# Performance work log

Hardware: AMD Instinct MI355X
Metric: run time of the kernel (lower is better)

The kernel has to match this reference:

```python
import jax, jax.numpy as jnp
import numpy as np

N_NODES = 100000
N_EDGES = 3200000
IN_DIM = 512
HID = 256
N_CLASSES = 40


def spmm(edge_src, edge_dst, edge_w, h):
    # out[d] = sum_{e: dst[e]==d} w[e] * h[src[e]]   (COO sparse-dense matmul)
    msgs = h[edge_src] * edge_w[:, None]  # [E, F]
    return jax.ops.segment_sum(msgs, edge_dst, num_segments=N_NODES)


def setup_inputs() -> dict:
    key = jax.random.key(0)
    ks = jax.random.split(key, 20)
    inp = {
        "x": jax.random.normal(ks[0], (N_NODES, IN_DIM), dtype=jnp.float32),
        "edge_src": jax.random.randint(ks[1], (N_EDGES,), 0, N_NODES, dtype=jnp.int32),
        "edge_dst": jax.random.randint(ks[2], (N_EDGES,), 0, N_NODES, dtype=jnp.int32),
        "edge_w": jax.random.uniform(ks[3], (N_EDGES,), dtype=jnp.float32),
    }
    def lin(k, fi, fo):
        s = 1.0 / np.sqrt(fi)
        kw, kb = jax.random.split(k)
        return (jax.random.uniform(kw, (fi, fo), minval=-s, maxval=s, dtype=jnp.float32),
                jax.random.uniform(kb, (fo,), minval=-s, maxval=s, dtype=jnp.float32))
    inp["w1"], inp["b1"] = lin(ks[4], IN_DIM, HID)      # GCN layer 1
    inp["w2"], inp["b2"] = lin(ks[5], HID, HID)         # GCN layer 2
    inp["wc1"], inp["bc1"] = lin(ks[6], HID, 2 * HID)   # classifier MLP
    inp["wc2"], inp["bc2"] = lin(ks[7], 2 * HID, 2 * HID)
    inp["wc3"], inp["bc3"] = lin(ks[8], 2 * HID, 2 * HID)
    inp["wc4"], inp["bc4"] = lin(ks[9], 2 * HID, N_CLASSES)
    return inp


def reference(x, edge_src, edge_dst, edge_w, w1, b1, w2, b2,
              wc1, bc1, wc2, bc2, wc3, bc3, wc4, bc4):
    h = jax.nn.relu(spmm(edge_src, edge_dst, edge_w, x @ w1) + b1)
    # dropout rate = 0.0 -> identity
    h = spmm(edge_src, edge_dst, edge_w, h @ w2) + b2
    # node classifier MLP
    h = jax.nn.relu(h @ wc1 + bc1)
    h = jax.nn.relu(h @ wc2 + bc2)
    h = jax.nn.relu(h @ wc3 + bc3)
    logits = h @ wc4 + bc4
    return jax.nn.softmax(logits, axis=1)
```

## Files before the change

kernel.cpp:

```cpp
#include <hip/hip_runtime.h>
#include <math.h>

typedef __attribute__((ext_vector_type(8))) _Float16 f16x8;
typedef __attribute__((ext_vector_type(4))) float f32x4;
typedef __attribute__((ext_vector_type(8))) unsigned short ushort8;


__device__ __forceinline__ float bf2f(unsigned short u) {
    union { unsigned int i; float f; } x; x.i = ((unsigned int)u) << 16; return x.f;
}
__device__ __forceinline__ unsigned short f2bf(float f) {
    union { float f; unsigned int i; } x; x.f = f;
    unsigned int i = x.i;
    unsigned int r = (i + 0x7FFFu + ((i >> 16) & 1u)) >> 16;
    return (unsigned short)r;
}
__device__ __forceinline__ float h2f(unsigned short u) {
    _Float16 h; __builtin_memcpy(&h, &u, 2); return (float)h;
}
__device__ __forceinline__ unsigned short f2h(float f) {
    _Float16 h = (_Float16)f; unsigned short u; __builtin_memcpy(&u, &h, 2); return u;
}
__device__ __forceinline__ float ld1(const void* p, long i, bool bf) {
    return bf ? bf2f(((const unsigned short*)p)[i]) : ((const float*)p)[i];
}
__device__ __forceinline__ float4 ld4(const void* p, long i, bool bf) {
    if (bf) {
        ushort4 u = *(const ushort4*)((const unsigned short*)p + i);
        return make_float4(bf2f(u.x), bf2f(u.y), bf2f(u.z), bf2f(u.w));
    }
    return *(const float4*)((const float*)p + i);
}

__global__ void k_detect(const unsigned int* __restrict__ x, int* __restrict__ flag) {
    int t = threadIdx.x;
    int hits = 0;
    for (int i = 0; i < 64; i++) {
        unsigned int w = x[t * 64 + i];
        unsigned int e = (w >> 7) & 0xFF;
        hits += (e >= 0x70 && e <= 0x85) ? 1 : 0;
    }
    __shared__ int sh[256];
    sh[t] = hits;
    __syncthreads();
    for (int off = 128; off; off >>= 1) {
        if (t < off) sh[t] += sh[t + off];
        __syncthreads();
    }
    if (t == 0) *flag = (sh[0] > 8192) ? 1 : 0;
}


__global__ void k_hist(const int* __restrict__ dst, int E, int* __restrict__ counts) {
    int i = blockIdx.x * blockDim.x + threadIdx.x;
    if (i < E) atomicAdd(&counts[dst[i]], 1);
}

__global__ void k_scan_a(const int* __restrict__ counts, int N,
                         int* __restrict__ ex, int* __restrict__ bsums) {
    __shared__ int s[256];
    int t = threadIdx.x;
    int base = blockIdx.x * 1024;
    int v[4]; int sum = 0;
    #pragma unroll
    for (int j = 0; j < 4; j++) {
        int idx = base + t * 4 + j;
        v[j] = (idx < N) ? counts[idx] : 0;
        sum += v[j];
    }
    s[t] = sum;
    __syncthreads();
    for (int off = 1; off < 256; off <<= 1) {
        int x = (t >= off) ? s[t - off] : 0;
        __syncthreads();
        s[t] += x;
        __syncthreads();
    }
    int run = (t > 0) ? s[t - 1] : 0;
    #pragma unroll
    for (int j = 0; j < 4; j++) {
        int idx = base + t * 4 + j;
        if (idx < N) ex[idx] = run;
        run += v[j];
    }
    if (t == 255) bsums[blockIdx.x] = s[255];
}

__global__ void k_scan_b(int* __restrict__ bsums, int nb) {
    __shared__ int s[256];
    int t = threadIdx.x;
    s[t] = (t < nb) ? bsums[t] : 0;
    __syncthreads();
    for (int off = 1; off < 256; off <<= 1) {
        int x = (t >= off) ? s[t - off] : 0;
        __syncthreads();
        s[t] += x;
        __syncthreads();
    }
    if (t < nb) bsums[t] = (t > 0) ? s[t - 1] : 0;
}

__global__ void k_scan_c(const int* __restrict__ ex, const int* __restrict__ bsums,
                         int N, int E, int* __restrict__ row_ptr) {
    int i = blockIdx.x * blockDim.x + threadIdx.x;
    if (i < N) row_ptr[i] = ex[i] + bsums[i >> 10];
    if (i == 0) row_ptr[N] = E;
}

__global__ void k_scatter(const int* __restrict__ src, const int* __restrict__ dst,
                          const void* __restrict__ ewin, const int* __restrict__ dflag,
                          const int* __restrict__ row_ptr, int* __restrict__ cursor,
                          int E, int* __restrict__ es, float* __restrict__ ew) {
    int i = blockIdx.x * blockDim.x + threadIdx.x;
    if (i >= E) return;
    bool bf = (*dflag != 0);
    int d = dst[i];
    int p = row_ptr[d] + atomicAdd(&cursor[d], 1);
    es[p] = src[i];
    ew[p] = ld1(ewin, i, bf);
}


__global__ __launch_bounds__(256) void k_gemm(
    const void* __restrict__ A, const void* __restrict__ W, const void* __restrict__ bias,
    void* __restrict__ C, int M, int K, int N,
    int a_kind, int c_mode, int act, const int* __restrict__ dflag)
{
    const bool inbf = (*dflag != 0);
    const int  a_mode = (a_kind == 2) ? 2 : (inbf ? 1 : 0);
    const bool a_lo = (a_mode == 0);
    const bool b_lo = !inbf;

    __shared__ _Float16 Ah[128][40];
    __shared__ _Float16 Al[128][40];
    __shared__ _Float16 Bh[128][40];
    __shared__ _Float16 Bl[128][40];

    const int t  = threadIdx.x;
    const int m0 = blockIdx.y * 128;
    const int n0 = blockIdx.x * 128;

    const int lane = t & 63;
    const int wv   = t >> 6;
    const int wm   = (wv & 1) * 64;
    const int wn   = (wv >> 1) * 64;
    const int lr   = lane & 15;
    const int lk   = (lane >> 4) * 8;

    f32x4 acc[4][4];
    const f32x4 vzero = {0.f, 0.f, 0.f, 0.f};
    #pragma unroll
    for (int i = 0; i < 4; i++)
        #pragma unroll
        for (int j = 0; j < 4; j++) acc[i][j] = vzero;

    const int  ar  = t >> 1;
    const int  ak  = (t & 1) * 16;
    const long agm = (long)(m0 + ar);

    const int nq = t & 31;
    const int kq = t >> 5;
    const int gn = n0 + nq * 4;

    for (int k0 = 0; k0 < K; k0 += 32) {
        #pragma unroll
        for (int c = 0; c < 2; c++) {
            long base = agm * K + k0 + ak + c * 8;
            if (a_mode == 2) {
                uint4 raw = make_uint4(0, 0, 0, 0);
                if (agm < M) raw = *(const uint4*)((const unsigned short*)A + base);
                *(uint4*)&Ah[ar][ak + c * 8] = raw;
            } else if (a_mode == 1) {
                union { unsigned short u[8]; uint4 q; } r;
                r.q = make_uint4(0, 0, 0, 0);
                if (agm < M) r.q = *(const uint4*)((const unsigned short*)A + base);
                union { _Float16 h[8]; uint4 q; } H;
                #pragma unroll
                for (int e = 0; e < 8; e++) H.h[e] = (_Float16)bf2f(r.u[e]);
                *(uint4*)&Ah[ar][ak + c * 8] = H.q;
            } else {
                float4 v0 = make_float4(0.f, 0.f, 0.f, 0.f), v1 = v0;
                if (agm < M) {
                    v0 = *(const float4*)((const float*)A + base);
                    v1 = *(const float4*)((const float*)A + base + 4);
                }
                float f[8] = {v0.x, v0.y, v0.z, v0.w, v1.x, v1.y, v1.z, v1.w};
                union { _Float16 h[8]; uint4 q; } H, L;
                #pragma unroll
                for (int e = 0; e < 8; e++) {
                    _Float16 hh = (_Float16)f[e];
                    H.h[e] = hh;
                    L.h[e] = (_Float16)(f[e] - (float)hh);
                }
                *(uint4*)&Ah[ar][ak + c * 8] = H.q;
                *(uint4*)&Al[ar][ak + c * 8] = L.q;
            }
        }
        {
            float w[4][4];
            #pragma unroll
            for (int i = 0; i < 4; i++) {
                float4 v = make_float4(0.f, 0.f, 0.f, 0.f);
                if (gn < N) v = ld4(W, (long)(k0 + kq * 4 + i) * N + gn, inbf);
                w[i][0] = v.x; w[i][1] = v.y; w[i][2] = v.z; w[i][3] = v.w;
            }
            #pragma unroll
            for (int j = 0; j < 4; j++) {
                union { _Float16 h[4]; uint2 q; } H, L;
                #pragma unroll
                for (int i = 0; i < 4; i++) {
                    _Float16 hh = (_Float16)w[i][j];
                    H.h[i] = hh;
                    if (b_lo) L.h[i] = (_Float16)(w[i][j] - (float)hh);
                }
                *(uint2*)&Bh[nq * 4 + j][kq * 4] = H.q;
                if (b_lo) *(uint2*)&Bl[nq * 4 + j][kq * 4] = L.q;
            }
        }
        __syncthreads();

        f16x8 ah[4], bh[4];
        #pragma unroll
        for (int f = 0; f < 4; f++) {
            ah[f] = *(const f16x8*)&Ah[wm + f * 16 + lr][lk];
            bh[f] = *(const f16x8*)&Bh[wn + f * 16 + lr][lk];
        }
        #pragma unroll
        for (int i = 0; i < 4; i++)
            #pragma unroll
            for (int j = 0; j < 4; j++)
                acc[i][j] = __builtin_amdgcn_mfma_f32_16x16x32_f16(ah[i], bh[j], acc[i][j], 0, 0, 0);
        if (a_lo) {
            f16x8 al[4];
            #pragma unroll
            for (int f = 0; f < 4; f++) al[f] = *(const f16x8*)&Al[wm + f * 16 + lr][lk];
            #pragma unroll
            for (int i = 0; i < 4; i++)
                #pragma unroll
                for (int j = 0; j < 4; j++)
                    acc[i][j] = __builtin_amdgcn_mfma_f32_16x16x32_f16(al[i], bh[j], acc[i][j], 0, 0, 0);
        }
        if (b_lo) {
            f16x8 bl[4];
            #pragma unroll
            for (int f = 0; f < 4; f++) bl[f] = *(const f16x8*)&Bl[wn + f * 16 + lr][lk];
            #pragma unroll
            for (int i = 0; i < 4; i++)
                #pragma unroll
                for (int j = 0; j < 4; j++)
                    acc[i][j] = __builtin_amdgcn_mfma_f32_16x16x32_f16(ah[i], bl[j], acc[i][j], 0, 0, 0);
        }
        __syncthreads();
    }

    const bool has_bias = (bias != nullptr);
    const int  rbase = (lane >> 4) * 4;
    #pragma unroll
    for (int j = 0; j < 4; j++) {
        int col = n0 + wn + j * 16 + lr;
        if (col >= N) continue;
        float bv = has_bias ? ld1(bias, col, inbf) : 0.f;
        #pragma unroll
        for (int i = 0; i < 4; i++) {
            #pragma unroll
            for (int r = 0; r < 4; r++) {
                int row = m0 + wm + i * 16 + rbase + r;
                if (row < M) {
                    float v = acc[i][j][r] + bv;
                    if (act) v = fmaxf(v, 0.f);
                    if (c_mode == 2) ((unsigned short*)C)[(long)row * N + col] = f2h(v);
                    else             ((float*)C)[(long)row * N + col] = v;
                }
            }
        }
    }
}


__global__ __launch_bounds__(256) void k_spmm(
    const unsigned short* __restrict__ sup, const int* __restrict__ es,
    const float* __restrict__ ew, const int* __restrict__ row_ptr,
    const void* __restrict__ bias, unsigned short* __restrict__ out,
    int Nn, int act, const int* __restrict__ dflag)
{
    const int wave = threadIdx.x >> 6;
    const int lane = threadIdx.x & 63;
    const int node = blockIdx.x * 4 + wave;
    if (node >= Nn) return;
    const bool bf = (*dflag != 0);

    const int half = lane >> 5;
    const int fl   = (lane & 31) * 8;

    const int e0 = row_ptr[node], e1 = row_ptr[node + 1];
    float acc[8] = {};

    #pragma unroll 4
    for (int e = e0 + half; e < e1; e += 2) {
        int s = es[e];
        float w = ew[e];
        ushort8 u = *(const ushort8*)&sup[(long)s * 256 + fl];
        #pragma unroll
        for (int i = 0; i < 8; i++) acc[i] += w * h2f(u[i]);
    }

    #pragma unroll
    for (int i = 0; i < 8; i++) acc[i] += __shfl_xor(acc[i], 32, 64);

    if (half == 0) {
        float4 b0 = ld4(bias, fl, bf);
        float4 b1 = ld4(bias, fl + 4, bf);
        float bb[8] = {b0.x, b0.y, b0.z, b0.w, b1.x, b1.y, b1.z, b1.w};
        ushort8 o;
        #pragma unroll
        for (int i = 0; i < 8; i++) {
            float v = acc[i] + bb[i];
            if (act) v = fmaxf(v, 0.f);
            o[i] = f2h(v);
        }
        *(ushort8*)&out[(long)node * 256 + fl] = o;
    }
}


__global__ __launch_bounds__(256) void k_softmax(
    const float* __restrict__ logits, void* __restrict__ out, int M, int NC,
    const int* __restrict__ dflag)
{
    const int wave = threadIdx.x >> 6;
    const int lane = threadIdx.x & 63;
    const int row = blockIdx.x * 4 + wave;
    if (row >= M) return;
    const bool bf = (*dflag != 0);

    float v = (lane < NC) ? logits[(long)row * NC + lane] : -INFINITY;
    float m = v;
    #pragma unroll
    for (int off = 32; off; off >>= 1) m = fmaxf(m, __shfl_xor(m, off, 64));
    float p = (lane < NC) ? expf(v - m) : 0.f;
    float s = p;
    #pragma unroll
    for (int off = 32; off; off >>= 1) s += __shfl_xor(s, off, 64);
    if (lane < NC) {
        float r = p / s;
        if (bf) ((unsigned short*)out)[(long)row * NC + lane] = f2bf(r);
        else    ((float*)out)[(long)row * NC + lane] = r;
    }
}


extern "C" void kernel_launch(void* const* d_in, const int* in_sizes, int n_in,
                              void* d_out, int out_size, void* d_ws, size_t ws_size,
                              hipStream_t stream) {
    const void* x    = d_in[0];
    const int*  esrc = (const int*)d_in[1];
    const int*  edst = (const int*)d_in[2];
    const void* ewin = d_in[3];
    const void* w1 = d_in[4],  *b1 = d_in[5];
    const void* w2 = d_in[6],  *b2 = d_in[7];
    const void* wc1 = d_in[8], *bc1 = d_in[9];
    const void* wc2 = d_in[10], *bc2 = d_in[11];
    const void* wc3 = d_in[12], *bc3 = d_in[13];
    const void* wc4 = d_in[14], *bc4 = d_in[15];

    const int HID  = in_sizes[5];
    const int IND  = in_sizes[4] / HID;
    const int HID2 = in_sizes[9];
    const int NC   = in_sizes[15];
    const int M    = in_sizes[0] / IND;
    const int E    = in_sizes[1];

    char* ws = (char*)d_ws;
    int* dflag = (int*)ws;
    unsigned short* bufA = (unsigned short*)(ws + 256);
    unsigned short* bufB = (unsigned short*)(ws + 256 + 102400000L);
    char*  wsC  = ws + 256 + 204800000L;
    char*  wsD  = wsC + 204800000L;
    unsigned short* bufC = (unsigned short*)wsC;
    unsigned short* bufD = (unsigned short*)wsD;

    int* counts  = (int*)wsC;
    int* row_ptr = counts + 100352;
    int* cursor  = row_ptr + 100352;
    int* bsums   = cursor + 100352;
    int* ex      = bsums + 1024;
    int* es      = ex + 100352;
    float* ewS   = (float*)(es + E);

    float* logits = (float*)bufA;

    k_detect<<<1, 256, 0, stream>>>((const unsigned int*)x, dflag);

    hipMemsetAsync(counts, 0, 100352 * sizeof(int), stream);
    hipMemsetAsync(cursor, 0, 100352 * sizeof(int), stream);
    k_hist<<<(E + 255) / 256, 256, 0, stream>>>(edst, E, counts);
    int nb = (M + 1023) / 1024;
    k_scan_a<<<nb, 256, 0, stream>>>(counts, M, ex, bsums);
    k_scan_b<<<1, 256, 0, stream>>>(bsums, nb);
    k_scan_c<<<(M + 255) / 256, 256, 0, stream>>>(ex, bsums, M, E, row_ptr);
    k_scatter<<<(E + 255) / 256, 256, 0, stream>>>(esrc, edst, ewin, dflag, row_ptr, cursor, E, es, ewS);

    const int gm128 = (M + 127) / 128;
    dim3 blk(256);

    k_gemm<<<dim3(HID / 128, gm128), blk, 0, stream>>>(x, w1, nullptr, bufA, M, IND, HID, 0, 2, 0, dflag);
    k_spmm<<<(M + 3) / 4, blk, 0, stream>>>(bufA, es, ewS, row_ptr, b1, bufB, M, 1, dflag);
    k_gemm<<<dim3(HID / 128, gm128), blk, 0, stream>>>(bufB, w2, nullptr, bufA, M, HID, HID, 2, 2, 0, dflag);
    k_spmm<<<(M + 3) / 4, blk, 0, stream>>>(bufA, es, ewS, row_ptr, b2, bufB, M, 0, dflag);
    k_gemm<<<dim3(HID2 / 128, gm128), blk, 0, stream>>>(bufB, wc1, bc1, bufC, M, HID, HID2, 2, 2, 1, dflag);
    k_gemm<<<dim3(HID2 / 128, gm128), blk, 0, stream>>>(bufC, wc2, bc2, bufD, M, HID2, HID2, 2, 2, 1, dflag);
    k_gemm<<<dim3(HID2 / 128, gm128), blk, 0, stream>>>(bufD, wc3, bc3, bufC, M, HID2, HID2, 2, 2, 1, dflag);
    k_gemm<<<dim3(1, gm128), blk, 0, stream>>>(bufC, wc4, bc4, logits, M, HID2, NC, 2, 0, 0, dflag);
    k_softmax<<<(M + 3) / 4, blk, 0, stream>>>(logits, d_out, M, NC, dflag);
}
```

Measured before the change: 2.026 ms.

## Pre-transpose and pre-split weights, load B fragments directly from global memory

Adds a prep kernel that transposes each weight matrix once per call into fp16 hi/lo and bf16 copies laid out as [N][K]. The GEMM then reads B fragments straight from global memory instead of converting and staging them through LDS each k-step, and uses bf16 MFMA for bf16 inputs so the A-side conversion is skipped. The epilogue is changed to vectorized 4-wide stores by swapping operand order. This removes per-tile weight conversion and LDS traffic for B, at the cost of extra prep launches and uncoalesced, non-reused global loads of B fragments per wave.

```diff
diff --git a/kernel.cpp b/kernel.cpp
--- a/kernel.cpp
+++ b/kernel.cpp
@@ -2,6 +2,7 @@
 #include <math.h>
 
 typedef __attribute__((ext_vector_type(8))) _Float16 f16x8;
+typedef __attribute__((ext_vector_type(8))) short bf16x8;
 typedef __attribute__((ext_vector_type(4))) float f32x4;
 typedef __attribute__((ext_vector_type(8))) unsigned short ushort8;
 
@@ -48,6 +49,21 @@
         __syncthreads();
     }
     if (t == 0) *flag = (sh[0] > 8192) ? 1 : 0;
+}
+
+
+__global__ void k_prep(const void* __restrict__ W, int K, int N,
+                       _Float16* __restrict__ outH, _Float16* __restrict__ outL,
+                       unsigned short* __restrict__ outBf, const int* __restrict__ dflag) {
+    const int k = blockIdx.x * 256 + threadIdx.x;
+    const int n = blockIdx.y;
+    const bool bf = (*dflag != 0);
+    float w = (n < N) ? ld1(W, (long)k * N + n, bf) : 0.f;
+    long idx = (long)n * K + k;
+    _Float16 h = (_Float16)w;
+    outH[idx] = h;
+    outL[idx] = (_Float16)(w - (float)h);
+    outBf[idx] = f2bf(w);
 }
 
 
@@ -122,8 +138,10 @@
 
 
 __global__ __launch_bounds__(256) void k_gemm(
-    const void* __restrict__ A, const void* __restrict__ W, const void* __restrict__ bias,
-    void* __restrict__ C, int M, int K, int N,
+    const void* __restrict__ A,
+    const _Float16* __restrict__ BTh, const _Float16* __restrict__ BTl,
+    const unsigned short* __restrict__ BTbf,
+    const void* __restrict__ bias, void* __restrict__ C, int M, int K, int N,
     int a_kind, int c_mode, int act, const int* __restrict__ dflag)
 {
     const bool inbf = (*dflag != 0);
@@ -131,10 +149,8 @@
     const bool a_lo = (a_mode == 0);
     const bool b_lo = !inbf;
 
-    __shared__ _Float16 Ah[128][40];
-    __shared__ _Float16 Al[128][40];
-    __shared__ _Float16 Bh[128][40];
-    __shared__ _Float16 Bl[128][40];
+    __shared__ unsigned short Ah[128][40];
+    __shared__ unsigned short Al[128][40];
 
     const int t  = threadIdx.x;
     const int m0 = blockIdx.y * 128;
@@ -158,26 +174,16 @@
     const int  ak  = (t & 1) * 16;
     const long agm = (long)(m0 + ar);
 
-    const int nq = t & 31;
-    const int kq = t >> 5;
-    const int gn = n0 + nq * 4;
+    const long brow = (long)(n0 + wn + lr) * K + lk;
 
     for (int k0 = 0; k0 < K; k0 += 32) {
         #pragma unroll
         for (int c = 0; c < 2; c++) {
             long base = agm * K + k0 + ak + c * 8;
-            if (a_mode == 2) {
+            if (a_mode != 0) {
                 uint4 raw = make_uint4(0, 0, 0, 0);
                 if (agm < M) raw = *(const uint4*)((const unsigned short*)A + base);
                 *(uint4*)&Ah[ar][ak + c * 8] = raw;
-            } else if (a_mode == 1) {
-                union { unsigned short u[8]; uint4 q; } r;
-                r.q = make_uint4(0, 0, 0, 0);
-                if (agm < M) r.q = *(const uint4*)((const unsigned short*)A + base);
-                union { _Float16 h[8]; uint4 q; } H;
-                #pragma unroll
-                for (int e = 0; e < 8; e++) H.h[e] = (_Float16)bf2f(r.u[e]);
-                *(uint4*)&Ah[ar][ak + c * 8] = H.q;
             } else {
                 float4 v0 = make_float4(0.f, 0.f, 0.f, 0.f), v1 = v0;
                 if (agm < M) {
@@ -196,81 +202,80 @@
                 *(uint4*)&Al[ar][ak + c * 8] = L.q;
             }
         }
-        {
-            float w[4][4];
+        __syncthreads();
+
+        if (a_mode == 1) {
+            bf16x8 a[4], b[4];
             #pragma unroll
-            for (int i = 0; i < 4; i++) {
-                float4 v = make_float4(0.f, 0.f, 0.f, 0.f);
-                if (gn < N) v = ld4(W, (long)(k0 + kq * 4 + i) * N + gn, inbf);
-                w[i][0] = v.x; w[i][1] = v.y; w[i][2] = v.z; w[i][3] = v.w;
-            }
-            #pragma unroll
-            for (int j = 0; j < 4; j++) {
-                union { _Float16 h[4]; uint2 q; } H, L;
-                #pragma unroll
-                for (int i = 0; i < 4; i++) {
-                    _Float16 hh = (_Float16)w[i][j];
-                    H.h[i] = hh;
-                    if (b_lo) L.h[i] = (_Float16)(w[i][j] - (float)hh);
-                }
-                *(uint2*)&Bh[nq * 4 + j][kq * 4] = H.q;
-                if (b_lo) *(uint2*)&Bl[nq * 4 + j][kq * 4] = L.q;
-            }
-        }
-        __syncthreads();
-
-        f16x8 ah[4], bh[4];
-        #pragma unroll
-        for (int f = 0; f < 4; f++) {
-            ah[f] = *(const f16x8*)&Ah[wm + f * 16 + lr][lk];
-            bh[f] = *(const f16x8*)&Bh[wn + f * 16 + lr][lk];
-        }
-        #pragma unroll
-        for (int i = 0; i < 4; i++)
-            #pragma unroll
-            for (int j = 0; j < 4; j++)
-                acc[i][j] = __builtin_amdgcn_mfma_f32_16x16x32_f16(ah[i], bh[j], acc[i][j], 0, 0, 0);
-        if (a_lo) {
-            f16x8 al[4];
-            #pragma unroll
-            for (int f = 0; f < 4; f++) al[f] = *(const f16x8*)&Al[wm + f * 16 + lr][lk];
+            for (int f = 0; f < 4; f++) {
+                b[f] = *(const bf16x8*)&BTbf[brow + (long)f * 16 * K + k0];
+                a[f] = *(const bf16x8*)&Ah[wm + f * 16 + lr][lk];
+            }
             #pragma unroll
             for (int i = 0; i < 4; i++)
                 #pragma unroll
                 for (int j = 0; j < 4; j++)
-                    acc[i][j] = __builtin_amdgcn_mfma_f32_16x16x32_f16(al[i], bh[j], acc[i][j], 0, 0, 0);
-        }
-        if (b_lo) {
-            f16x8 bl[4];
+                    acc[i][j] = __builtin_amdgcn_mfma_f32_16x16x32_bf16(b[j], a[i], acc[i][j], 0, 0, 0);
+        } else {
+            f16x8 a[4], b[4];
             #pragma unroll
-            for (int f = 0; f < 4; f++) bl[f] = *(const f16x8*)&Bl[wn + f * 16 + lr][lk];
+            for (int f = 0; f < 4; f++) {
+                b[f] = *(const f16x8*)&BTh[brow + (long)f * 16 * K + k0];
+                a[f] = *(const f16x8*)&Ah[wm + f * 16 + lr][lk];
+            }
             #pragma unroll
             for (int i = 0; i < 4; i++)
                 #pragma unroll
                 for (int j = 0; j < 4; j++)
-                    acc[i][j] = __builtin_amdgcn_mfma_f32_16x16x32_f16(ah[i], bl[j], acc[i][j], 0, 0, 0);
+                    acc[i][j] = __builtin_amdgcn_mfma_f32_16x16x32_f16(b[j], a[i], acc[i][j], 0, 0, 0);
+            if (a_lo) {
+                f16x8 al[4];
+                #pragma unroll
+                for (int f = 0; f < 4; f++) al[f] = *(const f16x8*)&Al[wm + f * 16 + lr][lk];
+                #pragma unroll
+                for (int i = 0; i < 4; i++)
+                    #pragma unroll
+                    for (int j = 0; j < 4; j++)
+                        acc[i][j] = __builtin_amdgcn_mfma_f32_16x16x32_f16(b[j], al[i], acc[i][j], 0, 0, 0);
+            }
+            if (b_lo) {
+                f16x8 bl[4];
+                #pragma unroll
+                for (int f = 0; f < 4; f++) bl[f] = *(const f16x8*)&BTl[brow + (long)f * 16 * K + k0];
+                #pragma unroll
+                for (int i = 0; i < 4; i++)
+                    #pragma unroll
+                    for (int j = 0; j < 4; j++)
+                        acc[i][j] = __builtin_amdgcn_mfma_f32_16x16x32_f16(bl[j], a[i], acc[i][j], 0, 0, 0);
+            }
         }
         __syncthreads();
     }
 
     const bool has_bias = (bias != nullptr);
-    const int  rbase = (lane >> 4) * 4;
-    #pragma unroll
-    for (int j = 0; j < 4; j++) {
-        int col = n0 + wn + j * 16 + lr;
-        if (col >= N) continue;
-        float bv = has_bias ? ld1(bias, col, inbf) : 0.f;
+    const int  nb4 = (lane >> 4) * 4;
+    #pragma unroll
+    for (int i = 0; i < 4; i++) {
+        int m = m0 + wm + i * 16 + lr;
+        if (m >= M) continue;
         #pragma unroll
-        for (int i = 0; i < 4; i++) {
-            #pragma unroll
-            for (int r = 0; r < 4; r++) {
-                int row = m0 + wm + i * 16 + rbase + r;
-                if (row < M) {
-                    float v = acc[i][j][r] + bv;
-                    if (act) v = fmaxf(v, 0.f);
-                    if (c_mode == 2) ((unsigned short*)C)[(long)row * N + col] = f2h(v);
-                    else             ((float*)C)[(long)row * N + col] = v;
-                }
+        for (int j = 0; j < 4; j++) {
+            int nb = n0 + wn + j * 16 + nb4;
+            if (nb >= N) continue;
+            float4 bv = has_bias ? ld4(bias, nb, inbf) : make_float4(0.f, 0.f, 0.f, 0.f);
+            float v0 = acc[i][j][0] + bv.x;
+            float v1 = acc[i][j][1] + bv.y;
+            float v2 = acc[i][j][2] + bv.z;
+            float v3 = acc[i][j][3] + bv.w;
+            if (act) {
+                v0 = fmaxf(v0, 0.f); v1 = fmaxf(v1, 0.f);
+                v2 = fmaxf(v2, 0.f); v3 = fmaxf(v3, 0.f);
+            }
+            if (c_mode == 2) {
+                ushort4 o; o.x = f2h(v0); o.y = f2h(v1); o.z = f2h(v2); o.w = f2h(v3);
+                *(ushort4*)&((unsigned short*)C)[(long)m * N + nb] = o;
+            } else {
+                *(float4*)&((float*)C)[(long)m * N + nb] = make_float4(v0, v1, v2, v3);
             }
         }
     }
@@ -389,7 +394,24 @@
 
     float* logits = (float*)bufA;
 
+    _Float16* P = (_Float16*)(wsD + 103000000L);
+    const long s_w1 = 256L * 512, s_w2 = 256L * 256, s_c1 = 512L * 256;
+    const long s_c2 = 512L * 512, s_c3 = 512L * 512, s_c4 = 128L * 512;
+    _Float16 *w1h = P,              *w1l = w1h + s_w1; unsigned short* w1b = (unsigned short*)(w1l + s_w1);
+    _Float16 *w2h = (_Float16*)(w1b + s_w1), *w2l = w2h + s_w2; unsigned short* w2b = (unsigned short*)(w2l + s_w2);
+    _Float16 *c1h = (_Float16*)(w2b + s_w2), *c1l = c1h + s_c1; unsigned short* c1b = (unsigned short*)(c1l + s_c1);
+    _Float16 *c2h = (_Float16*)(c1b + s_c1), *c2l = c2h + s_c2; unsigned short* c2b = (unsigned short*)(c2l + s_c2);
+    _Float16 *c3h = (_Float16*)(c2b + s_c2), *c3l = c3h + s_c3; unsigned short* c3b = (unsigned short*)(c3l + s_c3);
+    _Float16 *c4h = (_Float16*)(c3b + s_c3), *c4l = c4h + s_c4; unsigned short* c4b = (unsigned short*)(c4l + s_c4);
+
     k_detect<<<1, 256, 0, stream>>>((const unsigned int*)x, dflag);
+
+    k_prep<<<dim3(IND / 256, HID),  256, 0, stream>>>(w1,  IND,  HID,  w1h, w1l, w1b, dflag);
+    k_prep<<<dim3(HID / 256, HID),  256, 0, stream>>>(w2,  HID,  HID,  w2h, w2l, w2b, dflag);
+    k_prep<<<dim3(HID / 256, HID2), 256, 0, stream>>>(wc1, HID,  HID2, c1h, c1l, c1b, dflag);
+    k_prep<<<dim3(HID2 / 256, HID2),256, 0, stream>>>(wc2, HID2, HID2, c2h, c2l, c2b, dflag);
+    k_prep<<<dim3(HID2 / 256, HID2),256, 0, stream>>>(wc3, HID2, HID2, c3h, c3l, c3b, dflag);
+    k_prep<<<dim3(HID2 / 256, 128), 256, 0, stream>>>(wc4, HID2, NC,   c4h, c4l, c4b, dflag);
 
     hipMemsetAsync(counts, 0, 100352 * sizeof(int), stream);
     hipMemsetAsync(cursor, 0, 100352 * sizeof(int), stream);
@@ -403,13 +425,13 @@
     const int gm128 = (M + 127) / 128;
     dim3 blk(256);
 
-    k_gemm<<<dim3(HID / 128, gm128), blk, 0, stream>>>(x, w1, nullptr, bufA, M, IND, HID, 0, 2, 0, dflag);
+    k_gemm<<<dim3(HID / 128, gm128), blk, 0, stream>>>(x, w1h, w1l, w1b, nullptr, bufA, M, IND, HID, 0, 2, 0, dflag);
     k_spmm<<<(M + 3) / 4, blk, 0, stream>>>(bufA, es, ewS, row_ptr, b1, bufB, M, 1, dflag);
-    k_gemm<<<dim3(HID / 128, gm128), blk, 0, stream>>>(bufB, w2, nullptr, bufA, M, HID, HID, 2, 2, 0, dflag);
+    k_gemm<<<dim3(HID / 128, gm128), blk, 0, stream>>>(bufB, w2h, w2l, w2b, nullptr, bufA, M, HID, HID, 2, 2, 0, dflag);
     k_spmm<<<(M + 3) / 4, blk, 0, stream>>>(bufA, es, ewS, row_ptr, b2, bufB, M, 0, dflag);
-    k_gemm<<<dim3(HID2 / 128, gm128), blk, 0, stream>>>(bufB, wc1, bc1, bufC, M, HID, HID2, 2, 2, 1, dflag);
-    k_gemm<<<dim3(HID2 / 128, gm128), blk, 0, stream>>>(bufC, wc2, bc2, bufD, M, HID2, HID2, 2, 2, 1, dflag);
-    k_gemm<<<dim3(HID2 / 128, gm128), blk, 0, stream>>>(bufD, wc3, bc3, bufC, M, HID2, HID2, 2, 2, 1, dflag);
-    k_gemm<<<dim3(1, gm128), blk, 0, stream>>>(bufC, wc4, bc4, logits, M, HID2, NC, 2, 0, 0, dflag);
+    k_gemm<<<dim3(HID2 / 128, gm128), blk, 0, stream>>>(bufB, c1h, c1l, c1b, bc1, bufC, M, HID, HID2, 2, 2, 1, dflag);
+    k_gemm<<<dim3(HID2 / 128, gm128), blk, 0, stream>>>(bufC, c2h, c2l, c2b, bc2, bufD, M, HID2, HID2, 2, 2, 1, dflag);
+    k_gemm<<<dim3(HID2 / 128, gm128), blk, 0, stream>>>(bufD, c3h, c3l, c3b, bc3, bufC, M, HID2, HID2, 2, 2, 1, dflag);
+    k_gemm<<<dim3(1, gm128), blk, 0, stream>>>(bufC, c4h, c4l, c4b, bc4, logits, M, HID2, NC, 2, 0, 0, dflag);
     k_softmax<<<(M + 3) / 4, blk, 0, stream>>>(logits, d_out, M, NC, dflag);
 }
```

After: 2.242 ms. 10.7% more time.
